# Performance work log

Hardware: AMD Instinct MI355X
Metric: run time of the kernel (lower is better)

## Reference

```python
import jax, jax.numpy as jnp
import numpy as np

N_BLOCKS = 16
BLOCK_SIZE = 512
TOP_K = N_BLOCKS // 4  # matches n_blocks // 4 in the source


def setup_inputs() -> dict:
    key = jax.random.key(0)
    k1, k2, k3, k4, k5 = jax.random.split(key, 5)
    in_f, out_f = 2048, 8192
    x = jax.random.normal(k1, (2, 4096, in_f), dtype=jnp.float32)
    # router: Linear(in_features, n_blocks)
    Wr = jax.random.normal(k2, (N_BLOCKS, in_f), dtype=jnp.float32) * (in_f ** -0.5)
    br = jnp.zeros((N_BLOCKS,), dtype=jnp.float32)
    # fc1: Linear(in, out); fc2: Linear(out, in). Biases are unused in the original forward.
    W1 = jax.random.normal(k3, (out_f, in_f), dtype=jnp.float32) * (in_f ** -0.5)
    W2 = jax.random.normal(k4, (in_f, out_f), dtype=jnp.float32) * (out_f ** -0.5)
    return {"x": x, "Wr": Wr, "br": br, "W1": W1, "W2": W2}


def reference(x, Wr, br, W1, W2):
    x_shape = x.shape
    in_f = x_shape[-1]
    xf = x.reshape(-1, in_f)                      # [N, in]
    n = xf.shape[0]
    # router + top-k block selection per token
    prob = jax.nn.softmax(xf @ Wr.T + br, axis=-1)          # [N, nb]
    _, idx = jax.lax.top_k(prob, TOP_K)                      # [N, k]
    mask = jnp.zeros((n, N_BLOCKS), dtype=xf.dtype)
    mask = mask.at[jnp.arange(n)[:, None], idx].set(1.0)     # [N, nb]
    # fc1 per block: h[n,i,b] = x @ W1_block_i^T  (bias never used in source)
    W1b = W1.reshape(N_BLOCKS, BLOCK_SIZE, in_f)
    h = jnp.einsum('nf,ibf->nib', xf, W1b)                   # [N, nb, bs]
    # activation, then zero out unselected blocks (unselected never reach fc2)
    h = jax.nn.gelu(h, approximate=False) * mask[:, :, None]
    # fc2 per block accumulate: y = sum_i h_i @ W2_block_i^T
    W2b = W2.reshape(in_f, N_BLOCKS, BLOCK_SIZE)
    y = jnp.einsum('nib,fib->nf', h, W2b)                    # [N, in]
    return y.reshape(x_shape)
```

## Files before the change

kernel.cpp:

```cpp
#include <hip/hip_runtime.h>
#include <hip/hip_bf16.h>

#define N_TOK 8192
#define IN_F  2048
#define OUT_F 8192
#define NB    16
#define BS    512
#define BM2   256
#define MAX_MT2 144

typedef short          bf16x8  __attribute__((ext_vector_type(8)));
typedef unsigned short ushort8 __attribute__((ext_vector_type(8)));
typedef float          f32x4   __attribute__((ext_vector_type(4)));
typedef _Float16       f16x8   __attribute__((ext_vector_type(8)));

#define WS_COUNTS 0
#define WS_TSTART 64
#define WS_SEL    256
#define WS_INV    (32*1024)
#define WS_LISTS  (192*1024)
#define WS_XBF    (1ull<<20)
#define WS_W2BF   WS_XBF
#define WS_H      (WS_XBF + 33554432ull)
#define WS_W1BF   (WS_H + 37748736ull)
#define WS_YP     WS_W1BF

static __device__ __forceinline__ unsigned short f2bf(float f) {
    __hip_bfloat16 h = __float2bfloat16(f);
    return *reinterpret_cast<unsigned short*>(&h);
}

static __device__ __forceinline__ void gload16(const unsigned short* g, unsigned short* lds) {
    __builtin_amdgcn_global_load_lds(
        (const __attribute__((address_space(1))) unsigned int*)g,
        (__attribute__((address_space(3))) unsigned int*)lds, 16, 0, 0);
}

#define MFMA16(ai, bi) \
    acc[0][0] = __builtin_amdgcn_mfma_f32_16x16x32_bf16(ai##0, bi##0, acc[0][0], 0, 0, 0); \
    acc[0][1] = __builtin_amdgcn_mfma_f32_16x16x32_bf16(ai##0, bi##1, acc[0][1], 0, 0, 0); \
    acc[0][2] = __builtin_amdgcn_mfma_f32_16x16x32_bf16(ai##0, bi##2, acc[0][2], 0, 0, 0); \
    acc[0][3] = __builtin_amdgcn_mfma_f32_16x16x32_bf16(ai##0, bi##3, acc[0][3], 0, 0, 0); \
    acc[1][0] = __builtin_amdgcn_mfma_f32_16x16x32_bf16(ai##1, bi##0, acc[1][0], 0, 0, 0); \
    acc[1][1] = __builtin_amdgcn_mfma_f32_16x16x32_bf16(ai##1, bi##1, acc[1][1], 0, 0, 0); \
    acc[1][2] = __builtin_amdgcn_mfma_f32_16x16x32_bf16(ai##1, bi##2, acc[1][2], 0, 0, 0); \
    acc[1][3] = __builtin_amdgcn_mfma_f32_16x16x32_bf16(ai##1, bi##3, acc[1][3], 0, 0, 0); \
    acc[2][0] = __builtin_amdgcn_mfma_f32_16x16x32_bf16(ai##2, bi##0, acc[2][0], 0, 0, 0); \
    acc[2][1] = __builtin_amdgcn_mfma_f32_16x16x32_bf16(ai##2, bi##1, acc[2][1], 0, 0, 0); \
    acc[2][2] = __builtin_amdgcn_mfma_f32_16x16x32_bf16(ai##2, bi##2, acc[2][2], 0, 0, 0); \
    acc[2][3] = __builtin_amdgcn_mfma_f32_16x16x32_bf16(ai##2, bi##3, acc[2][3], 0, 0, 0); \
    acc[3][0] = __builtin_amdgcn_mfma_f32_16x16x32_bf16(ai##3, bi##0, acc[3][0], 0, 0, 0); \
    acc[3][1] = __builtin_amdgcn_mfma_f32_16x16x32_bf16(ai##3, bi##1, acc[3][1], 0, 0, 0); \
    acc[3][2] = __builtin_amdgcn_mfma_f32_16x16x32_bf16(ai##3, bi##2, acc[3][2], 0, 0, 0); \
    acc[3][3] = __builtin_amdgcn_mfma_f32_16x16x32_bf16(ai##3, bi##3, acc[3][3], 0, 0, 0);

#define PHASE_TAIL \
    __builtin_amdgcn_s_barrier(); \
    asm volatile("s_waitcnt lgkmcnt(0)" ::: "memory"); \
    __builtin_amdgcn_sched_barrier(0); \
    __builtin_amdgcn_s_setprio(1); \
    MFMA16(a, b) \
    __builtin_amdgcn_s_setprio(0); \
    __builtin_amdgcn_sched_barrier(0); \
    __builtin_amdgcn_s_barrier();

__global__ __launch_bounds__(256) void router_kernel(
    const float* __restrict__ x, const float* __restrict__ Wr,
    const float* __restrict__ br, unsigned short* __restrict__ sel)
{
    const int tid = threadIdx.x;
    const int lt = tid & 63;
    const int wv = tid >> 6;
    const int tok = blockIdx.x * 4 + wv;
    const int e = lt >> 2, p = lt & 3;
    const float4* xp = (const float4*)(x + (size_t)tok * IN_F);
    const float4* wp = (const float4*)(Wr + (size_t)e * IN_F);
    double s = 0.0;
    for (int j = p; j < IN_F / 4; j += 4) {
        float4 a = xp[j], w = wp[j];
        s += (double)a.x * w.x + (double)a.y * w.y + (double)a.z * w.z + (double)a.w * w.w;
    }
    s += __shfl_down(s, 2);
    s += __shfl_down(s, 1);
    __shared__ double logits[4][NB];
    if (p == 0) logits[wv][e] = s + (double)br[e];
    __syncthreads();
    if (lt == 0) {
        unsigned used = 0, packed = 0;
        #pragma unroll
        for (int kk = 0; kk < 4; ++kk) {
            int best = 0; double bv = -1.0e300;
            #pragma unroll
            for (int i = 0; i < NB; ++i)
                if (!((used >> i) & 1u) && logits[wv][i] > bv) { bv = logits[wv][i]; best = i; }
            used |= 1u << best;
            packed |= (unsigned)best << (4 * kk);
        }
        sel[tok] = (unsigned short)packed;
    }
}

__global__ __launch_bounds__(256) void build_lists_kernel(
    const unsigned short* __restrict__ sel, int* __restrict__ counts,
    int* __restrict__ lists, unsigned* __restrict__ inv)
{
    const int e = blockIdx.x;
    const int t = threadIdx.x;
    unsigned short mysel[N_TOK / 256];
    int cnt = 0;
    #pragma unroll
    for (int i = 0; i < N_TOK / 256; ++i) {
        unsigned s = sel[i * 256 + t];
        mysel[i] = (unsigned short)s;
        bool m = ((s & 15u) == (unsigned)e) | (((s >> 4) & 15u) == (unsigned)e) |
                 (((s >> 8) & 15u) == (unsigned)e) | (((s >> 12) & 15u) == (unsigned)e);
        cnt += m ? 1 : 0;
    }
    __shared__ int ps[256];
    ps[t] = cnt;
    __syncthreads();
    #pragma unroll
    for (int off = 1; off < 256; off <<= 1) {
        int v = (t >= off) ? ps[t - off] : 0;
        __syncthreads();
        ps[t] += v;
        __syncthreads();
    }
    int pos = ps[t] - cnt;
    if (t == 255) counts[e] = ps[255];
    #pragma unroll
    for (int i = 0; i < N_TOK / 256; ++i) {
        unsigned s = mysel[i];
        bool m = ((s & 15u) == (unsigned)e) | (((s >> 4) & 15u) == (unsigned)e) |
                 (((s >> 8) & 15u) == (unsigned)e) | (((s >> 12) & 15u) == (unsigned)e);
        if (m) {
            const int tok = i * 256 + t;
            int j = ((s & 15u) == (unsigned)e) ? 0 :
                    (((s >> 4) & 15u) == (unsigned)e) ? 1 :
                    (((s >> 8) & 15u) == (unsigned)e) ? 2 : 3;
            inv[tok * 4 + j] = ((unsigned)e << 16) | (unsigned)pos;
            lists[e * N_TOK + pos++] = tok;
        }
    }
}

__global__ void scan_kernel(const int* __restrict__ counts, int* __restrict__ tstart)
{
    if (threadIdx.x == 0) {
        int acc = 0;
        for (int i = 0; i < NB; ++i) { tstart[i] = acc; acc += (counts[i] + BM2 - 1) / BM2; }
        tstart[NB] = acc;
    }
}

__global__ __launch_bounds__(256) void convert_swz_kernel(
    const float* __restrict__ src, unsigned short* __restrict__ dst, int sh)
{
    const int total = 1 << 21;
    for (int id = blockIdx.x * 256 + threadIdx.x; id < total; id += 2048 * 256) {
        const int row = id >> sh;
        const int sr  = id & ((1 << sh) - 1);
        const int ps  = sr ^ (row & 7);
        const float4* s4 = (const float4*)(src + ((size_t)id << 3));
        float4 p0 = s4[0], p1 = s4[1];
        ushort8 o;
        o[0] = f2bf(p0.x); o[1] = f2bf(p0.y); o[2] = f2bf(p0.z); o[3] = f2bf(p0.w);
        o[4] = f2bf(p1.x); o[5] = f2bf(p1.y); o[6] = f2bf(p1.z); o[7] = f2bf(p1.w);
        *(ushort8*)(dst + (((size_t)(row) << sh) << 3) + ((size_t)ps << 3)) = o;
    }
}

__global__ __launch_bounds__(512) void fc1_kernel(
    const unsigned short* __restrict__ x_bf, const unsigned short* __restrict__ w1_bf,
    const int* __restrict__ lists, const int* __restrict__ counts,
    const int* __restrict__ tstart, unsigned short* __restrict__ h)
{
    __shared__ unsigned short lds[73728];
    const int bid = blockIdx.x;
    const int newid = (bid & 7) * 72 + (bid >> 3);
    const int nt = newid & 3, mt = newid >> 2;
    if (mt >= tstart[NB]) return;
    int b = 0;
    #pragma unroll
    for (int i = 1; i < NB; ++i) b += (mt >= tstart[i]);
    const int cnt  = counts[b];
    const int row0 = (mt - tstart[b]) * BM2;
    const int tid  = threadIdx.x;
    const int wave = tid >> 6, lane = tid & 63;
    const int sph = lane & 7;
    const int rbase = wave * 8 + (lane >> 3);

    const unsigned short* aS[4];
    const unsigned short* bS[2];
    #pragma unroll
    for (int i = 0; i < 4; ++i) {
        const int r = i * 64 + rbase;
        const int gr = min(row0 + r, cnt - 1);
        const int tok = lists[b * N_TOK + gr];
        aS[i] = x_bf + (size_t)tok * IN_F + ((sph ^ (r & 7) ^ (tok & 7)) << 3);
    }
    #pragma unroll
    for (int j = 0; j < 2; ++j) {
        const int r = j * 64 + rbase;
        bS[j] = w1_bf + (size_t)(b * BS + nt * 128 + r) * IN_F + (sph << 3);
    }
    const int wbase = wave * 512;

    const int lr16 = lane & 15, q = lane >> 4;
    const int wm = (wave >> 1) * 64, wn = (wave & 1) * 64;
    int offA[4], offB[4];
    #pragma unroll
    for (int i = 0; i < 4; ++i) { const int r = wm + i * 16 + lr16; offA[i] = r * 64 + ((q ^ (r & 7)) << 3); }
    #pragma unroll
    for (int j = 0; j < 4; ++j) { const int r = wn + j * 16 + lr16; offB[j] = r * 64 + ((q ^ (r & 7)) << 3); }

    f32x4 acc[4][4];
    #pragma unroll
    for (int i = 0; i < 4; ++i)
        #pragma unroll
        for (int j = 0; j < 4; ++j) acc[i][j] = (f32x4)0.0f;

#define STA1(k, buf, i) gload16(aS[i] + (size_t)(k) * 64, lds + (buf) * 24576 + (i) * 4096 + wbase)
#define STB1(k, buf, j) gload16(bS[j] + (size_t)(k) * 64, lds + (buf) * 24576 + 16384 + (j) * 4096 + wbase)

    STA1(0,0,0); STA1(0,0,1); STA1(0,0,2); STA1(0,0,3); STB1(0,0,0); STB1(0,0,1);
    STA1(1,1,0); STA1(1,1,1); STA1(1,1,2); STA1(1,1,3); STB1(1,1,0); STB1(1,1,1);
    asm volatile("s_waitcnt vmcnt(6)" ::: "memory");
    __builtin_amdgcn_s_barrier();

    const int NK = IN_F / 64;
    int cur = 0;
    for (int k = 0; k < NK; ++k) {
        const unsigned short* Ab = lds + cur * 24576;
        const unsigned short* Bb = Ab + 16384;
        const int nxt = (cur == 0) ? 2 : cur - 1;
        bf16x8 a0 = *(const bf16x8*)&Ab[offA[0]];
        bf16x8 a1 = *(const bf16x8*)&Ab[offA[1]];
        bf16x8 a2 = *(const bf16x8*)&Ab[offA[2]];
        bf16x8 a3 = *(const bf16x8*)&Ab[offA[3]];
        bf16x8 b0 = *(const bf16x8*)&Bb[offB[0]];
        bf16x8 b1 = *(const bf16x8*)&Bb[offB[1]];
        bf16x8 b2 = *(const bf16x8*)&Bb[offB[2]];
        bf16x8 b3 = *(const bf16x8*)&Bb[offB[3]];
        if (k + 2 < NK) { STA1(k + 2, nxt, 0); STA1(k + 2, nxt, 1); STB1(k + 2, nxt, 0); }
        PHASE_TAIL
        a0 = *(const bf16x8*)&Ab[offA[0] ^ 32];
        a1 = *(const bf16x8*)&Ab[offA[1] ^ 32];
        a2 = *(const bf16x8*)&Ab[offA[2] ^ 32];
        a3 = *(const bf16x8*)&Ab[offA[3] ^ 32];
        b0 = *(const bf16x8*)&Bb[offB[0] ^ 32];
        b1 = *(const bf16x8*)&Bb[offB[1] ^ 32];
        b2 = *(const bf16x8*)&Bb[offB[2] ^ 32];
        b3 = *(const bf16x8*)&Bb[offB[3] ^ 32];
        if (k + 2 < NK) {
            STA1(k + 2, nxt, 2); STA1(k + 2, nxt, 3); STB1(k + 2, nxt, 1);
            asm volatile("s_waitcnt vmcnt(6)" ::: "memory");
        } else if (k + 1 < NK) {
            asm volatile("s_waitcnt vmcnt(0)" ::: "memory");
        }
        PHASE_TAIL
        cur = (cur == 2) ? 0 : cur + 1;
    }
    #pragma unroll
    for (int i = 0; i < 4; ++i) {
        #pragma unroll
        for (int r = 0; r < 4; ++r) {
            const int lrow = wm + i * 16 + q * 4 + r;
            if (row0 + lrow < cnt) {
                const size_t hrow = (size_t)(mt * BM2 + lrow) * BS;
                const int r7 = (lrow & 7) << 3;
                #pragma unroll
                for (int j = 0; j < 4; ++j) {
                    const int col = nt * 128 + wn + j * 16 + lr16;
                    float v = acc[i][j][r];
                    v = 0.5f * v * (1.0f + erff(v * 0.70710678118654752f));
                    h[hrow + (col ^ r7)] = f2bf(v);
                }
            }
        }
    }
#undef STA1
#undef STB1
}

__global__ __launch_bounds__(512) void fc2_kernel(
    const unsigned short* __restrict__ h, const unsigned short* __restrict__ w2_bf,
    const int* __restrict__ counts, const int* __restrict__ tstart,
    _Float16* __restrict__ yp)
{
    __shared__ unsigned short lds[73728];
    const int bid = blockIdx.x;
    const int newid = (bid & 7) * 288 + (bid >> 3);
    const int nt = newid & 15, mt = newid >> 4;
    if (mt >= tstart[NB]) return;
    int b = 0;
    #pragma unroll
    for (int i = 1; i < NB; ++i) b += (mt >= tstart[i]);
    const int cnt  = counts[b];
    const int row0 = (mt - tstart[b]) * BM2;
    const int tid  = threadIdx.x;
    const int wave = tid >> 6, lane = tid & 63;
    const int sph = lane & 7;
    const int rbase = wave * 8 + (lane >> 3);

    const unsigned short* aS[4];
    const unsigned short* bS[2];
    #pragma unroll
    for (int i = 0; i < 4; ++i) {
        const int r = i * 64 + rbase;
        aS[i] = h + (size_t)(mt * BM2 + r) * BS + (sph << 3);
    }
    #pragma unroll
    for (int j = 0; j < 2; ++j) {
        const int r = j * 64 + rbase;
        bS[j] = w2_bf + (size_t)(nt * 128 + r) * OUT_F + b * BS + (sph << 3);
    }
    const int wbase = wave * 512;

    const int lr16 = lane & 15, q = lane >> 4;
    const int wm = (wave >> 1) * 64, wn = (wave & 1) * 64;
    int offA[4], offB[4];
    #pragma unroll
    for (int i = 0; i < 4; ++i) { const int r = wm + i * 16 + lr16; offA[i] = r * 64 + ((q ^ (r & 7)) << 3); }
    #pragma unroll
    for (int j = 0; j < 4; ++j) { const int r = wn + j * 16 + lr16; offB[j] = r * 64 + ((q ^ (r & 7)) << 3); }

    f32x4 acc[4][4];
    #pragma unroll
    for (int i = 0; i < 4; ++i)
        #pragma unroll
        for (int j = 0; j < 4; ++j) acc[i][j] = (f32x4)0.0f;

#define STA2(k, buf, i) gload16(aS[i] + (size_t)(k) * 64, lds + (buf) * 24576 + (i) * 4096 + wbase)
#define STB2(k, buf, j) gload16(bS[j] + (size_t)(k) * 64, lds + (buf) * 24576 + 16384 + (j) * 4096 + wbase)

    STA2(0,0,0); STA2(0,0,1); STA2(0,0,2); STA2(0,0,3); STB2(0,0,0); STB2(0,0,1);
    STA2(1,1,0); STA2(1,1,1); STA2(1,1,2); STA2(1,1,3); STB2(1,1,0); STB2(1,1,1);
    asm volatile("s_waitcnt vmcnt(6)" ::: "memory");
    __builtin_amdgcn_s_barrier();

    const int NK = BS / 64;
    int cur = 0;
    for (int k = 0; k < NK; ++k) {
        const unsigned short* Ab = lds + cur * 24576;
        const unsigned short* Bb = Ab + 16384;
        const int nxt = (cur == 0) ? 2 : cur - 1;
        bf16x8 a0 = *(const bf16x8*)&Ab[offA[0]];
        bf16x8 a1 = *(const bf16x8*)&Ab[offA[1]];
        bf16x8 a2 = *(const bf16x8*)&Ab[offA[2]];
        bf16x8 a3 = *(const bf16x8*)&Ab[offA[3]];
        bf16x8 b0 = *(const bf16x8*)&Bb[offB[0]];
        bf16x8 b1 = *(const bf16x8*)&Bb[offB[1]];
        bf16x8 b2 = *(const bf16x8*)&Bb[offB[2]];
        bf16x8 b3 = *(const bf16x8*)&Bb[offB[3]];
        if (k + 2 < NK) { STA2(k + 2, nxt, 0); STA2(k + 2, nxt, 1); STB2(k + 2, nxt, 0); }
        PHASE_TAIL
        a0 = *(const bf16x8*)&Ab[offA[0] ^ 32];
        a1 = *(const bf16x8*)&Ab[offA[1] ^ 32];
        a2 = *(const bf16x8*)&Ab[offA[2] ^ 32];
        a3 = *(const bf16x8*)&Ab[offA[3] ^ 32];
        b0 = *(const bf16x8*)&Bb[offB[0] ^ 32];
        b1 = *(const bf16x8*)&Bb[offB[1] ^ 32];
        b2 = *(const bf16x8*)&Bb[offB[2] ^ 32];
        b3 = *(const bf16x8*)&Bb[offB[3] ^ 32];
        if (k + 2 < NK) {
            STA2(k + 2, nxt, 2); STA2(k + 2, nxt, 3); STB2(k + 2, nxt, 1);
            asm volatile("s_waitcnt vmcnt(6)" ::: "memory");
        } else if (k + 1 < NK) {
            asm volatile("s_waitcnt vmcnt(0)" ::: "memory");
        }
        PHASE_TAIL
        cur = (cur == 2) ? 0 : cur + 1;
    }
    #pragma unroll
    for (int i = 0; i < 4; ++i) {
        #pragma unroll
        for (int r = 0; r < 4; ++r) {
            const int lrow = wm + i * 16 + q * 4 + r;
            if (row0 + lrow < cnt) {
                _Float16* yrow = yp + (size_t)(mt * BM2 + lrow) * IN_F + nt * 128 + wn + lr16;
                #pragma unroll
                for (int j = 0; j < 4; ++j)
                    yrow[j * 16] = (_Float16)acc[i][j][r];
            }
        }
    }
#undef STA2
#undef STB2
}

__global__ __launch_bounds__(256) void reduce_kernel(
    const _Float16* __restrict__ yp, const unsigned* __restrict__ inv,
    const int* __restrict__ tstart, float* __restrict__ y)
{
    const int tok = blockIdx.x;
    __shared__ size_t rbase[4];
    if (threadIdx.x < 4) {
        unsigned v = inv[tok * 4 + threadIdx.x];
        rbase[threadIdx.x] = (size_t)(tstart[v >> 16] * BM2 + (int)(v & 0xFFFFu)) * IN_F;
    }
    __syncthreads();
    const int c = threadIdx.x * 8;
    f16x8 v0 = *(const f16x8*)(yp + rbase[0] + c);
    f16x8 v1 = *(const f16x8*)(yp + rbase[1] + c);
    f16x8 v2 = *(const f16x8*)(yp + rbase[2] + c);
    f16x8 v3 = *(const f16x8*)(yp + rbase[3] + c);
    float out[8];
    #pragma unroll
    for (int j = 0; j < 8; ++j)
        out[j] = (float)v0[j] + (float)v1[j] + (float)v2[j] + (float)v3[j];
    float4* yo = (float4*)(y + (size_t)tok * IN_F + c);
    yo[0] = make_float4(out[0], out[1], out[2], out[3]);
    yo[1] = make_float4(out[4], out[5], out[6], out[7]);
}

extern "C" void kernel_launch(void* const* d_in, const int* in_sizes, int n_in,
                              void* d_out, int out_size, void* d_ws, size_t ws_size,
                              hipStream_t stream) {
    const float* x  = (const float*)d_in[0];
    const float* Wr = (const float*)d_in[1];
    const float* br = (const float*)d_in[2];
    const float* W1 = (const float*)d_in[3];
    const float* W2 = (const float*)d_in[4];
    float* y = (float*)d_out;
    char* ws = (char*)d_ws;
    int* counts = (int*)(ws + WS_COUNTS);
    int* tstart = (int*)(ws + WS_TSTART);
    unsigned short* sel = (unsigned short*)(ws + WS_SEL);
    unsigned* inv = (unsigned*)(ws + WS_INV);
    int* lists  = (int*)(ws + WS_LISTS);
    unsigned short* x_bf  = (unsigned short*)(ws + WS_XBF);
    unsigned short* w1_bf = (unsigned short*)(ws + WS_W1BF);
    unsigned short* w2_bf = (unsigned short*)(ws + WS_W2BF);
    unsigned short* h     = (unsigned short*)(ws + WS_H);
    _Float16* yp          = (_Float16*)(ws + WS_YP);

    hipLaunchKernelGGL(router_kernel, dim3(N_TOK / 4), dim3(256), 0, stream, x, Wr, br, sel);
    hipLaunchKernelGGL(build_lists_kernel, dim3(NB), dim3(256), 0, stream, sel, counts, lists, inv);
    hipLaunchKernelGGL(scan_kernel, dim3(1), dim3(64), 0, stream, counts, tstart);
    hipLaunchKernelGGL(convert_swz_kernel, dim3(2048), dim3(256), 0, stream, x,  x_bf,  8);
    hipLaunchKernelGGL(convert_swz_kernel, dim3(2048), dim3(256), 0, stream, W1, w1_bf, 8);
    hipLaunchKernelGGL(fc1_kernel, dim3(4 * MAX_MT2), dim3(512), 0, stream, x_bf, w1_bf, lists, counts, tstart, h);
    hipLaunchKernelGGL(convert_swz_kernel, dim3(2048), dim3(256), 0, stream, W2, w2_bf, 10);
    hipLaunchKernelGGL(fc2_kernel, dim3(16 * MAX_MT2), dim3(512), 0, stream, h, w2_bf, counts, tstart, yp);
    hipLaunchKernelGGL(reduce_kernel, dim3(N_TOK), dim3(256), 0, stream, yp, inv, tstart, y);
}
```

Measured before the change: 407.5 us.

## Enlarge fc2 output tile to 256x256 with double buffering and stage router input in LDS

The fc2 kernel now computes a 256x256 output tile per workgroup, with each wave holding 8x4 MFMA accumulators, instead of 256x128. The grid shrinks to 8 column tiles. The pipeline goes from a three-stage buffer to two LDS buffers with a full vmcnt(0) wait each k-step, aiming to halve the number of times A (h) is reloaded. The router kernel copies each token's x row into shared memory before the dot products. Risks are higher register pressure from 128 accumulator floats per lane, weaker latency hiding from the shallower pipeline, and fewer workgroups to fill the CUs.

```diff
diff --git a/kernel.cpp b/kernel.cpp
--- a/kernel.cpp
+++ b/kernel.cpp
@@ -68,16 +68,21 @@
     const float* __restrict__ x, const float* __restrict__ Wr,
     const float* __restrict__ br, unsigned short* __restrict__ sel)
 {
+    __shared__ float xs[4][IN_F];
     const int tid = threadIdx.x;
     const int lt = tid & 63;
     const int wv = tid >> 6;
     const int tok = blockIdx.x * 4 + wv;
+    float4* xl = (float4*)xs[wv];
+    const float4* xp = (const float4*)(x + (size_t)tok * IN_F);
+    #pragma unroll
+    for (int i = 0; i < 8; ++i) xl[lt + i * 64] = xp[lt + i * 64];
+    __syncthreads();
     const int e = lt >> 2, p = lt & 3;
-    const float4* xp = (const float4*)(x + (size_t)tok * IN_F);
     const float4* wp = (const float4*)(Wr + (size_t)e * IN_F);
     double s = 0.0;
     for (int j = p; j < IN_F / 4; j += 4) {
-        float4 a = xp[j], w = wp[j];
+        float4 a = xl[j], w = wp[j];
         s += (double)a.x * w.x + (double)a.y * w.y + (double)a.z * w.z + (double)a.w * w.w;
     }
     s += __shfl_down(s, 2);
@@ -288,10 +293,10 @@
     const int* __restrict__ counts, const int* __restrict__ tstart,
     _Float16* __restrict__ yp)
 {
-    __shared__ unsigned short lds[73728];
+    __shared__ unsigned short lds[2][32768];
     const int bid = blockIdx.x;
-    const int newid = (bid & 7) * 288 + (bid >> 3);
-    const int nt = newid & 15, mt = newid >> 4;
+    const int newid = (bid & 7) * 144 + (bid >> 3);
+    const int nt = newid & 7, mt = newid >> 3;
     if (mt >= tstart[NB]) return;
     int b = 0;
     #pragma unroll
@@ -304,89 +309,89 @@
     const int rbase = wave * 8 + (lane >> 3);
 
     const unsigned short* aS[4];
-    const unsigned short* bS[2];
-    #pragma unroll
-    for (int i = 0; i < 4; ++i) {
-        const int r = i * 64 + rbase;
-        aS[i] = h + (size_t)(mt * BM2 + r) * BS + (sph << 3);
-    }
-    #pragma unroll
-    for (int j = 0; j < 2; ++j) {
-        const int r = j * 64 + rbase;
-        bS[j] = w2_bf + (size_t)(nt * 128 + r) * OUT_F + b * BS + (sph << 3);
+    const unsigned short* bS[4];
+    #pragma unroll
+    for (int g = 0; g < 4; ++g) {
+        const int r = g * 64 + rbase;
+        aS[g] = h + (size_t)(mt * BM2 + r) * BS + (sph << 3);
+        bS[g] = w2_bf + (size_t)(nt * 256 + r) * OUT_F + b * BS + (sph << 3);
     }
     const int wbase = wave * 512;
 
     const int lr16 = lane & 15, q = lane >> 4;
-    const int wm = (wave >> 1) * 64, wn = (wave & 1) * 64;
-    int offA[4], offB[4];
-    #pragma unroll
-    for (int i = 0; i < 4; ++i) { const int r = wm + i * 16 + lr16; offA[i] = r * 64 + ((q ^ (r & 7)) << 3); }
-    #pragma unroll
-    for (int j = 0; j < 4; ++j) { const int r = wn + j * 16 + lr16; offB[j] = r * 64 + ((q ^ (r & 7)) << 3); }
-
-    f32x4 acc[4][4];
-    #pragma unroll
-    for (int i = 0; i < 4; ++i)
+    const int wr = (wave >> 2) * 128, wc = (wave & 3) * 64;
+    int offA[8], offB[4];
+    #pragma unroll
+    for (int i = 0; i < 8; ++i) { const int r = wr + i * 16 + lr16; offA[i] = r * 64 + ((q ^ (r & 7)) << 3); }
+    #pragma unroll
+    for (int j = 0; j < 4; ++j) { const int r = wc + j * 16 + lr16; offB[j] = 16384 + r * 64 + ((q ^ (r & 7)) << 3); }
+
+    f32x4 acc[8][4];
+    #pragma unroll
+    for (int i = 0; i < 8; ++i)
         #pragma unroll
         for (int j = 0; j < 4; ++j) acc[i][j] = (f32x4)0.0f;
 
-#define STA2(k, buf, i) gload16(aS[i] + (size_t)(k) * 64, lds + (buf) * 24576 + (i) * 4096 + wbase)
-#define STB2(k, buf, j) gload16(bS[j] + (size_t)(k) * 64, lds + (buf) * 24576 + 16384 + (j) * 4096 + wbase)
-
-    STA2(0,0,0); STA2(0,0,1); STA2(0,0,2); STA2(0,0,3); STB2(0,0,0); STB2(0,0,1);
-    STA2(1,1,0); STA2(1,1,1); STA2(1,1,2); STA2(1,1,3); STB2(1,1,0); STB2(1,1,1);
-    asm volatile("s_waitcnt vmcnt(6)" ::: "memory");
+#define ST2(k, buf) \
+    { _Pragma("unroll") for (int g = 0; g < 4; ++g) \
+        gload16(aS[g] + (size_t)(k) * 64, &lds[buf][g * 4096 + wbase]); \
+      _Pragma("unroll") for (int g = 0; g < 4; ++g) \
+        gload16(bS[g] + (size_t)(k) * 64, &lds[buf][16384 + g * 4096 + wbase]); }
+
+#define MFMA_8x4 \
+    __builtin_amdgcn_s_barrier(); \
+    asm volatile("s_waitcnt lgkmcnt(0)" ::: "memory"); \
+    __builtin_amdgcn_sched_barrier(0); \
+    __builtin_amdgcn_s_setprio(1); \
+    _Pragma("unroll") for (int i = 0; i < 8; ++i) \
+        _Pragma("unroll") for (int j = 0; j < 4; ++j) \
+            acc[i][j] = __builtin_amdgcn_mfma_f32_16x16x32_bf16(a[i], bb[j], acc[i][j], 0, 0, 0); \
+    __builtin_amdgcn_s_setprio(0); \
+    __builtin_amdgcn_sched_barrier(0); \
     __builtin_amdgcn_s_barrier();
 
+    ST2(0, 0);
+    asm volatile("s_waitcnt vmcnt(0)" ::: "memory");
+    __builtin_amdgcn_s_barrier();
+
     const int NK = BS / 64;
-    int cur = 0;
     for (int k = 0; k < NK; ++k) {
-        const unsigned short* Ab = lds + cur * 24576;
-        const unsigned short* Bb = Ab + 16384;
-        const int nxt = (cur == 0) ? 2 : cur - 1;
-        bf16x8 a0 = *(const bf16x8*)&Ab[offA[0]];
-        bf16x8 a1 = *(const bf16x8*)&Ab[offA[1]];
-        bf16x8 a2 = *(const bf16x8*)&Ab[offA[2]];
-        bf16x8 a3 = *(const bf16x8*)&Ab[offA[3]];
-        bf16x8 b0 = *(const bf16x8*)&Bb[offB[0]];
-        bf16x8 b1 = *(const bf16x8*)&Bb[offB[1]];
-        bf16x8 b2 = *(const bf16x8*)&Bb[offB[2]];
-        bf16x8 b3 = *(const bf16x8*)&Bb[offB[3]];
-        if (k + 2 < NK) { STA2(k + 2, nxt, 0); STA2(k + 2, nxt, 1); STB2(k + 2, nxt, 0); }
-        PHASE_TAIL
-        a0 = *(const bf16x8*)&Ab[offA[0] ^ 32];
-        a1 = *(const bf16x8*)&Ab[offA[1] ^ 32];
-        a2 = *(const bf16x8*)&Ab[offA[2] ^ 32];
-        a3 = *(const bf16x8*)&Ab[offA[3] ^ 32];
-        b0 = *(const bf16x8*)&Bb[offB[0] ^ 32];
-        b1 = *(const bf16x8*)&Bb[offB[1] ^ 32];
-        b2 = *(const bf16x8*)&Bb[offB[2] ^ 32];
-        b3 = *(const bf16x8*)&Bb[offB[3] ^ 32];
-        if (k + 2 < NK) {
-            STA2(k + 2, nxt, 2); STA2(k + 2, nxt, 3); STB2(k + 2, nxt, 1);
-            asm volatile("s_waitcnt vmcnt(6)" ::: "memory");
-        } else if (k + 1 < NK) {
-            asm volatile("s_waitcnt vmcnt(0)" ::: "memory");
-        }
-        PHASE_TAIL
-        cur = (cur == 2) ? 0 : cur + 1;
-    }
-    #pragma unroll
-    for (int i = 0; i < 4; ++i) {
+        const int cur = k & 1;
+        const unsigned short* L = lds[cur];
+        {
+            bf16x8 a[8], bb[4];
+            #pragma unroll
+            for (int i = 0; i < 8; ++i) a[i]  = *(const bf16x8*)&L[offA[i]];
+            #pragma unroll
+            for (int j = 0; j < 4; ++j) bb[j] = *(const bf16x8*)&L[offB[j]];
+            if (k + 1 < NK) ST2(k + 1, cur ^ 1);
+            MFMA_8x4
+        }
+        {
+            bf16x8 a[8], bb[4];
+            #pragma unroll
+            for (int i = 0; i < 8; ++i) a[i]  = *(const bf16x8*)&L[offA[i] ^ 32];
+            #pragma unroll
+            for (int j = 0; j < 4; ++j) bb[j] = *(const bf16x8*)&L[offB[j] ^ 32];
+            if (k + 1 < NK) asm volatile("s_waitcnt vmcnt(0)" ::: "memory");
+            MFMA_8x4
+        }
+    }
+    #pragma unroll
+    for (int i = 0; i < 8; ++i) {
         #pragma unroll
         for (int r = 0; r < 4; ++r) {
-            const int lrow = wm + i * 16 + q * 4 + r;
+            const int lrow = wr + i * 16 + q * 4 + r;
             if (row0 + lrow < cnt) {
-                _Float16* yrow = yp + (size_t)(mt * BM2 + lrow) * IN_F + nt * 128 + wn + lr16;
+                _Float16* yrow = yp + (size_t)(mt * BM2 + lrow) * IN_F + nt * 256 + wc + lr16;
                 #pragma unroll
                 for (int j = 0; j < 4; ++j)
                     yrow[j * 16] = (_Float16)acc[i][j][r];
             }
         }
     }
-#undef STA2
-#undef STB2
+#undef ST2
+#undef MFMA_8x4
 }
 
 __global__ __launch_bounds__(256) void reduce_kernel(
@@ -442,6 +447,6 @@
     hipLaunchKernelGGL(convert_swz_kernel, dim3(2048), dim3(256), 0, stream, W1, w1_bf, 8);
     hipLaunchKernelGGL(fc1_kernel, dim3(4 * MAX_MT2), dim3(512), 0, stream, x_bf, w1_bf, lists, counts, tstart, h);
     hipLaunchKernelGGL(convert_swz_kernel, dim3(2048), dim3(256), 0, stream, W2, w2_bf, 10);
-    hipLaunchKernelGGL(fc2_kernel, dim3(16 * MAX_MT2), dim3(512), 0, stream, h, w2_bf, counts, tstart, yp);
+    hipLaunchKernelGGL(fc2_kernel, dim3(8 * MAX_MT2), dim3(512), 0, stream, h, w2_bf, counts, tstart, yp);
     hipLaunchKernelGGL(reduce_kernel, dim3(N_TOK), dim3(256), 0, stream, yp, inv, tstart, y);
 }
```

New measurement: 409.3 us. About the same (+0.4%).
